# Kernel optimization log

Hardware: AMD Instinct MI355X
Metric: run time of the kernel (lower is better)

Reference implementation:

```python
import jax, jax.numpy as jnp
import numpy as np

IN_SIZE = 32
NUM_ACTIONS = 90
ACTION_DIM = 32
INNER_DIM = 256
HIDDEN_DIM = 512
N_LAYERS = 2
WORLD_STATE_SIZE = 32
# last 8 features are categorical (binary) flags, first 24 numeric
CAT_FLAGS = np.zeros(WORLD_STATE_SIZE, dtype=bool)
CAT_FLAGS[24:] = True


def setup_inputs() -> dict:
    key = jax.random.key(0)
    ks = jax.random.split(key, 20)
    s = 0.05
    b, t = 64, 512
    inp = {
        "batch_world_states_tensor": jax.random.normal(ks[0], (b, t, IN_SIZE), jnp.float32),
        "batch_action_indices": jax.random.randint(ks[1], (b, t), 0, NUM_ACTIONS),
        "action_emb": jax.random.normal(ks[2], (NUM_ACTIONS, ACTION_DIM), jnp.float32),
        "in_w": jax.random.normal(ks[3], (INNER_DIM - ACTION_DIM, IN_SIZE), jnp.float32) * s,
        "in_b": jax.random.normal(ks[4], (INNER_DIM - ACTION_DIM,), jnp.float32) * 0.005,
        "w_ih0": jax.random.normal(ks[5], (4 * HIDDEN_DIM, INNER_DIM), jnp.float32) * s,
        "w_hh0": jax.random.normal(ks[6], (4 * HIDDEN_DIM, HIDDEN_DIM), jnp.float32) * s,
        "b_ih0": jax.random.normal(ks[7], (4 * HIDDEN_DIM,), jnp.float32) * 0.005,
        "b_hh0": jax.random.normal(ks[8], (4 * HIDDEN_DIM,), jnp.float32) * 0.005,
        "w_ih1": jax.random.normal(ks[9], (4 * HIDDEN_DIM, HIDDEN_DIM), jnp.float32) * s,
        "w_hh1": jax.random.normal(ks[10], (4 * HIDDEN_DIM, HIDDEN_DIM), jnp.float32) * s,
        "b_ih1": jax.random.normal(ks[11], (4 * HIDDEN_DIM,), jnp.float32) * 0.005,
        "b_hh1": jax.random.normal(ks[12], (4 * HIDDEN_DIM,), jnp.float32) * 0.005,
        "out_w1": jax.random.normal(ks[13], (2 * HIDDEN_DIM, HIDDEN_DIM), jnp.float32) * s,
        "out_b1": jax.random.normal(ks[14], (2 * HIDDEN_DIM,), jnp.float32) * 0.005,
        "out_w2": jax.random.normal(ks[15], (WORLD_STATE_SIZE, 2 * HIDDEN_DIM), jnp.float32) * s,
        "out_b2": jax.random.normal(ks[16], (WORLD_STATE_SIZE,), jnp.float32) * 0.005,
    }
    return inp


def _lstm_layer(x, w_ih, w_hh, b_ih, b_hh):
    """x: [b, s, d_in] -> ([b, s, H], h_T, c_T). PyTorch gate order i,f,g,o."""
    b = x.shape[0]
    H = w_hh.shape[1]
    # precompute input-to-hidden contributions for all steps: [s, b, 4H]
    gx = jnp.einsum('bsd,gd->sbg', x, w_ih) + b_ih + b_hh
    h0 = jnp.zeros((b, H), x.dtype)
    c0 = jnp.zeros((b, H), x.dtype)

    def step(carry, g_t):
        h, c = carry
        g = g_t + h @ w_hh.T  # [b, 4H]
        i, f, gg, o = jnp.split(g, 4, axis=-1)
        i = jax.nn.sigmoid(i)
        f = jax.nn.sigmoid(f)
        gg = jnp.tanh(gg)
        o = jax.nn.sigmoid(o)
        c = f * c + i * gg
        h = o * jnp.tanh(c)
        return (h, c), h

    (hT, cT), hs = jax.lax.scan(step, (h0, c0), gx)
    return hs.transpose(1, 0, 2), hT, cT  # [b, s, H]


def reference(batch_world_states_tensor, batch_action_indices, action_emb,
              in_w, in_b, w_ih0, w_hh0, b_ih0, b_hh0,
              w_ih1, w_hh1, b_ih1, b_hh1,
              out_w1, out_b1, out_w2, out_b2):
    # input projection + action embedding concat
    proj = jax.nn.relu(jnp.einsum('bsd,ed->bse', batch_world_states_tensor, in_w) + in_b)
    acts = action_emb[batch_action_indices]  # [b, s, action_dim]
    x = jnp.concatenate([proj, acts], axis=-1)  # [b, s, inner_dim]
    # 2-layer LSTM
    x, h0T, c0T = _lstm_layer(x, w_ih0, w_hh0, b_ih0, b_hh0)
    rnn_out, h1T, c1T = _lstm_layer(x, w_ih1, w_hh1, b_ih1, b_hh1)
    # out projector
    hmid = jax.nn.relu(jnp.einsum('bsh,eh->bse', rnn_out, out_w1) + out_b1)
    out = jnp.einsum('bse,de->bsd', hmid, out_w2) + out_b2  # [b, s, D]
    # sigmoid on categorical feature slots
    cat_mask = jnp.asarray(CAT_FLAGS)
    out = jnp.where(cat_mask, jax.nn.sigmoid(out), out)
    return out[:, -1, :]  # [b, D]
```

## Files before the change

### kernel.cpp

```cpp
#include <hip/hip_runtime.h>

#define T_STEPS 512
#define BATCH   64
#define IN_SZ   32
#define AD      32
#define INNER   256
#define PROJ    224
#define HID     512
#define SENTW   0x7F7F7F7Fu
#define DEP     16
#define RST     6
#define SLOTW   4096

typedef __attribute__((ext_vector_type(8))) short short8;
typedef __attribute__((ext_vector_type(4))) float f32x4;
typedef __attribute__((ext_vector_type(4))) int   i32x4;

static __device__ __forceinline__ unsigned short f2bf(float f) {
  unsigned int u = __float_as_uint(f);
  u += 0x7FFFu + ((u >> 16) & 1u);
  return (unsigned short)(u >> 16);
}
static __device__ __forceinline__ float sigmoidf_(float x) { return 1.f / (1.f + __expf(-x)); }
static __device__ __forceinline__ float tanhf_(float x) {
  float e = __expf(-2.f * fabsf(x));
  float r = (1.f - e) / (1.f + e);
  return x < 0.f ? -r : r;
}

__global__ __launch_bounds__(256) void k_prep(
    const float* __restrict__ ws_in, const int* __restrict__ act_idx,
    const float* __restrict__ emb, const float* __restrict__ in_w,
    const float* __restrict__ in_b, unsigned short* __restrict__ x_bf)
{
  int t = blockIdx.x;
  int tid = threadIdx.x;
  __shared__ float st[BATCH * IN_SZ];
  __shared__ int ai[BATCH];
  for (int i = tid; i < BATCH * IN_SZ; i += 256) {
    int b = i >> 5, k = i & 31;
    st[i] = ws_in[((size_t)b * T_STEPS + t) * IN_SZ + k];
  }
  if (tid < BATCH) ai[tid] = act_idx[tid * T_STEPS + t];
  __syncthreads();
  if (tid < PROJ) {
    float w[IN_SZ];
    const float* wrow = in_w + tid * IN_SZ;
#pragma unroll
    for (int k = 0; k < IN_SZ; ++k) w[k] = wrow[k];
    float bb = in_b[tid];
    for (int b = 0; b < BATCH; ++b) {
      float acc = bb;
      const float* sb = st + b * IN_SZ;
#pragma unroll
      for (int k = 0; k < IN_SZ; ++k) acc += w[k] * sb[k];
      x_bf[((size_t)t * BATCH + b) * INNER + tid] = f2bf(fmaxf(acc, 0.f));
    }
  } else {
    int j = tid - PROJ;
    for (int b = 0; b < BATCH; ++b)
      x_bf[((size_t)t * BATCH + b) * INNER + tid] = f2bf(emb[ai[b] * AD + j]);
  }
}

static __device__ __forceinline__ short8 bfrag_load(const float* __restrict__ w, int stride, int row, int k0) {
  const float* p = w + (size_t)row * stride + k0;
  f32x4 a = *reinterpret_cast<const f32x4*>(p);
  f32x4 b = *reinterpret_cast<const f32x4*>(p + 4);
  short8 r;
  r[0] = (short)f2bf(a[0]); r[1] = (short)f2bf(a[1]); r[2] = (short)f2bf(a[2]); r[3] = (short)f2bf(a[3]);
  r[4] = (short)f2bf(b[0]); r[5] = (short)f2bf(b[1]); r[6] = (short)f2bf(b[2]); r[7] = (short)f2bf(b[3]);
  return r;
}

struct Frag64 { unsigned long long u[8]; };
union FU2 { unsigned long long u[2]; short8 s; };

static __device__ __forceinline__ void ld64(const unsigned long long* q, Frag64& f) {
#pragma unroll
  for (int kk = 0; kk < 4; ++kk) {
    f.u[kk * 2]     = __hip_atomic_load(q + kk * 128,     __ATOMIC_RELAXED, __HIP_MEMORY_SCOPE_AGENT);
    f.u[kk * 2 + 1] = __hip_atomic_load(q + kk * 128 + 1, __ATOMIC_RELAXED, __HIP_MEMORY_SCOPE_AGENT);
  }
}
static __device__ __forceinline__ bool fragok(const Frag64& f) {
  bool ok = true;
#pragma unroll
  for (int i = 0; i < 8; ++i)
    ok = ok & ((unsigned)(f.u[i] >> 32) != SENTW) & ((unsigned)f.u[i] != SENTW);
  return ok;
}

static __device__ __forceinline__ Frag64 poll_one(const unsigned long long* q) {
  Frag64 f;
  int miss = 0;
  while (true) {
    ld64(q, f);
    if (__all((int)fragok(f))) break;
    if (++miss > 2) __builtin_amdgcn_s_sleep(1);
  }
  return f;
}
static __device__ __forceinline__ void poll_two(const unsigned long long* qa, const unsigned long long* qb,
                                                Frag64& fa, Frag64& fb) {
  int miss = 0;
  while (true) {
    ld64(qa, fa);
    ld64(qb, fb);
    if (__all((int)(fragok(fa) & fragok(fb)))) break;
    if (++miss > 2) __builtin_amdgcn_s_sleep(1);
  }
}

static __device__ __forceinline__ void mfma4(const Frag64& f, const short8* wf, f32x4* acc) {
#pragma unroll
  for (int kk = 0; kk < 4; ++kk) {
    FU2 u; u.u[0] = f.u[kk * 2]; u.u[1] = f.u[kk * 2 + 1];
#pragma unroll
    for (int g = 0; g < 4; ++g)
      acc[g] = __builtin_amdgcn_mfma_f32_16x16x32_bf16(u.s, wf[g * 4 + kk], acc[g], 0, 0, 0);
  }
}

static __device__ __forceinline__ void st_agent(unsigned int* p, unsigned int v) {
  __hip_atomic_store(p, v, __ATOMIC_RELAXED, __HIP_MEMORY_SCOPE_AGENT);
}

static __device__ __forceinline__ size_t slotw(int bg, int d) { return ((size_t)(bg * DEP + d)) * SLOTW; }

template<int L>
static __device__ void lstm_body(
    const unsigned short* __restrict__ x_bf,
    const float* __restrict__ wih, const float* __restrict__ whh,
    const float* __restrict__ bih, const float* __restrict__ bhh,
    unsigned int* __restrict__ h0w, unsigned int* __restrict__ h1w,
    float* __restrict__ h1fin, unsigned int* __restrict__ flags,
    int bg, int blk, float* __restrict__ spart)
{
  constexpr int KI = (L == 0) ? 2 : 4;

  const int tid  = threadIdx.x;
  const int lane = tid & 63;
  const int wv   = tid >> 6;
  const int q    = lane >> 4;
  const int ln   = lane & 15;
  const int hid0 = blk << 4;
  const int m    = tid >> 4;
  const int n    = tid & 15;
  const int cb64 = (wv * 8 + (q >> 1)) * 64 + ln * 4 + (q & 1) * 2;

  float bias[4];
#pragma unroll
  for (int g = 0; g < 4; ++g)
    bias[g] = bih[g * HID + hid0 + n] + bhh[g * HID + hid0 + n];

  short8 fih[4 * KI];
#pragma unroll
  for (int g = 0; g < 4; ++g)
#pragma unroll
    for (int kk = 0; kk < KI; ++kk)
      fih[g * KI + kk] = bfrag_load(wih, (L == 0) ? INNER : HID,
                                    g * HID + hid0 + ln, (wv * KI + kk) * 32 + q * 8);
  short8 fhh[16];
#pragma unroll
  for (int g = 0; g < 4; ++g)
#pragma unroll
    for (int kk = 0; kk < 4; ++kk)
      fhh[g * 4 + kk] = bfrag_load(whh, HID, g * HID + hid0 + ln, (wv * 4 + kk) * 32 + q * 8);

  const int wo = blk * 128 + m * 8 + (n >> 1);
  float c_state = 0.f;

  for (int t = 0; t < T_STEPS; ++t) {
    f32x4 acc[4];
#pragma unroll
    for (int g = 0; g < 4; ++g) acc[g] = (f32x4){0.f, 0.f, 0.f, 0.f};

    if constexpr (L == 0) {
      const unsigned short* xr = x_bf + ((size_t)t * BATCH + bg * 16 + ln) * INNER + q * 8;
#pragma unroll
      for (int kk = 0; kk < KI; ++kk) {
        short8 xa = *reinterpret_cast<const short8*>(xr + (wv * KI + kk) * 32);
#pragma unroll
        for (int g = 0; g < 4; ++g)
          acc[g] = __builtin_amdgcn_mfma_f32_16x16x32_bf16(xa, fih[g * KI + kk], acc[g], 0, 0, 0);
      }
      if ((t & 3) == 0 && t >= 8) {
        const unsigned int* fp = flags + (bg * 32 + (lane & 31)) * 32;
        unsigned int tgt = (unsigned)(t - 4);
        while (true) {
          unsigned int v = __hip_atomic_load(fp, __ATOMIC_RELAXED, __HIP_MEMORY_SCOPE_AGENT);
          if (__all((int)(v >= tgt))) break;
          __builtin_amdgcn_s_sleep(1);
        }
        asm volatile("" ::: "memory");
      }
      if (t > 0) {
        Frag64 f = poll_one(reinterpret_cast<const unsigned long long*>(h0w + slotw(bg, (t - 1) & (DEP - 1))) + cb64);
        mfma4(f, fhh, acc);
      }
    } else {
      if (t > 0) {
        Frag64 fa, fb;
        poll_two(reinterpret_cast<const unsigned long long*>(h1w + slotw(bg, (t - 1) & (DEP - 1))) + cb64,
                 reinterpret_cast<const unsigned long long*>(h0w + slotw(bg, t & (DEP - 1))) + cb64, fa, fb);
        mfma4(fa, fhh, acc);
        mfma4(fb, fih, acc);
      } else {
        Frag64 fb = poll_one(reinterpret_cast<const unsigned long long*>(h0w + slotw(bg, 0)) + cb64);
        mfma4(fb, fih, acc);
      }
    }

    float* sp_w = spart + (t & 1) * 4096;
#pragma unroll
    for (int g = 0; g < 4; ++g)
#pragma unroll
      for (int r = 0; r < 4; ++r)
        sp_w[(((wv * 4 + g) * 4 + r) * 4 + (q ^ r)) * 16 + ln] = acc[g][r];
    __syncthreads();

    if constexpr (L == 1) {
      if ((t & 1) == 1 && tid == 0)
        st_agent(flags + (bg * 32 + blk) * 32, (unsigned)(t + 1));
    }

    float gate[4];
#pragma unroll
    for (int g = 0; g < 4; ++g) {
      float s = bias[g];
#pragma unroll
      for (int w2 = 0; w2 < 4; ++w2)
        s += sp_w[(((w2 * 4 + g) * 4 + (m & 3)) * 4 + ((m >> 2) ^ (m & 3))) * 16 + n];
      gate[g] = s;
    }
    float gi = sigmoidf_(gate[0]);
    float gf = sigmoidf_(gate[1]);
    float gc = tanhf_(gate[2]);
    float go = sigmoidf_(gate[3]);
    c_state = gf * c_state + gi * gc;
    float h = go * tanhf_(c_state);

    float hp = __shfl_xor(h, 1);
    unsigned int wword = (unsigned)f2bf(h) | ((unsigned)f2bf(hp) << 16);
    if constexpr (L == 0) {
      if (!(n & 1)) {
        st_agent(h0w + slotw(bg, t & (DEP - 1)) + wo, wword);
        st_agent(h0w + slotw(bg, (t + RST) & (DEP - 1)) + wo, SENTW);
      }
    } else {
      if (!(n & 1)) {
        st_agent(h1w + slotw(bg, t & (DEP - 1)) + wo, wword);
        st_agent(h1w + slotw(bg, (t + RST) & (DEP - 1)) + wo, SENTW);
      }
      if (t == T_STEPS - 1)
        h1fin[(size_t)(bg * 16 + m) * HID + hid0 + n] = h;
    }
  }
}

__global__ __launch_bounds__(256, 1) void k_lstm(
    const unsigned short* __restrict__ x_bf,
    const float* __restrict__ w_ih0, const float* __restrict__ w_hh0,
    const float* __restrict__ b_ih0, const float* __restrict__ b_hh0,
    const float* __restrict__ w_ih1, const float* __restrict__ w_hh1,
    const float* __restrict__ b_ih1, const float* __restrict__ b_hh1,
    unsigned int* h0w, unsigned int* h1w, float* h1fin, unsigned int* flags)
{
  __shared__ float spart[2 * 4096];
  const int xg  = blockIdx.x & 7;
  const int blk = blockIdx.x >> 3;
  const int bg  = xg & 3;
  if (xg < 4)
    lstm_body<0>(x_bf, w_ih0, w_hh0, b_ih0, b_hh0, h0w, h1w, h1fin, flags, bg, blk, spart);
  else
    lstm_body<1>(x_bf, w_ih1, w_hh1, b_ih1, b_hh1, h0w, h1w, h1fin, flags, bg, blk, spart);
}

__global__ __launch_bounds__(256) void k_head(
    const float* __restrict__ h1, const float* __restrict__ w1, const float* __restrict__ b1,
    const float* __restrict__ w2, const float* __restrict__ b2, float* __restrict__ out)
{
  int b = blockIdx.x, tid = threadIdx.x;
  __shared__ float sh[HID];
  __shared__ float sm[2 * HID];
  for (int k = tid; k < HID; k += 256) sh[k] = h1[(size_t)b * HID + k];
  __syncthreads();
#pragma unroll
  for (int r0 = 0; r0 < 4; ++r0) {
    int row = r0 * 256 + tid;
    const f32x4* wr = reinterpret_cast<const f32x4*>(w1 + (size_t)row * HID);
    float s = 0.f;
#pragma unroll 4
    for (int k = 0; k < HID / 4; ++k) {
      f32x4 v = wr[k];
      s += v[0] * sh[k * 4] + v[1] * sh[k * 4 + 1] + v[2] * sh[k * 4 + 2] + v[3] * sh[k * 4 + 3];
    }
    sm[row] = fmaxf(b1[row] + s, 0.f);
  }
  __syncthreads();
  if (tid < 32) {
    const f32x4* wr = reinterpret_cast<const f32x4*>(w2 + (size_t)tid * 2 * HID);
    float s = b2[tid];
#pragma unroll 4
    for (int k = 0; k < 2 * HID / 4; ++k) {
      f32x4 v = wr[k];
      s += v[0] * sm[k * 4] + v[1] * sm[k * 4 + 1] + v[2] * sm[k * 4 + 2] + v[3] * sm[k * 4 + 3];
    }
    if (tid >= 24) s = sigmoidf_(s);
    out[b * 32 + tid] = s;
  }
}

extern "C" void kernel_launch(void* const* d_in, const int* in_sizes, int n_in,
                              void* d_out, int out_size, void* d_ws, size_t ws_size,
                              hipStream_t stream) {
  const float* ws_in  = (const float*)d_in[0];
  const int*   aidx   = (const int*)d_in[1];
  const float* emb    = (const float*)d_in[2];
  const float* in_w   = (const float*)d_in[3];
  const float* in_b   = (const float*)d_in[4];
  const float* w_ih0  = (const float*)d_in[5];
  const float* w_hh0  = (const float*)d_in[6];
  const float* b_ih0  = (const float*)d_in[7];
  const float* b_hh0  = (const float*)d_in[8];
  const float* w_ih1  = (const float*)d_in[9];
  const float* w_hh1  = (const float*)d_in[10];
  const float* b_ih1  = (const float*)d_in[11];
  const float* b_hh1  = (const float*)d_in[12];
  const float* out_w1 = (const float*)d_in[13];
  const float* out_b1 = (const float*)d_in[14];
  const float* out_w2 = (const float*)d_in[15];
  const float* out_b2 = (const float*)d_in[16];

  unsigned char* ws = (unsigned char*)d_ws;
  const size_t X_OFF   = 0;
  const size_t RING_SZ = 4u * DEP * SLOTW * 4;
  const size_t H0_OFF  = 16777216;
  const size_t H1_OFF  = H0_OFF + RING_SZ;
  const size_t HF_OFF  = H1_OFF + RING_SZ;
  const size_t FL_OFF  = HF_OFF + 131072;
  unsigned short* x_bf  = (unsigned short*)(ws + X_OFF);
  unsigned int*   h0w   = (unsigned int*)(ws + H0_OFF);
  unsigned int*   h1w   = (unsigned int*)(ws + H1_OFF);
  float*          h1fin = (float*)(ws + HF_OFF);
  unsigned int*   flags = (unsigned int*)(ws + FL_OFF);

  hipMemsetAsync(ws + H0_OFF, 0x7F, 2 * RING_SZ, stream);
  hipMemsetAsync(ws + FL_OFF, 0, 16384, stream);
  k_prep<<<dim3(T_STEPS), dim3(256), 0, stream>>>(ws_in, aidx, emb, in_w, in_b, x_bf);
  k_lstm<<<dim3(256), dim3(256), 0, stream>>>(x_bf, w_ih0, w_hh0, b_ih0, b_hh0,
                                              w_ih1, w_hh1, b_ih1, b_hh1,
                                              h0w, h1w, h1fin, flags);
  k_head<<<dim3(BATCH), dim3(256), 0, stream>>>(h1fin, out_w1, out_b1, out_w2, out_b2, (float*)d_out);
}
```

Before: 1.494 ms.

## Poll per-wave step counters before reading LSTM hidden-state data

Each wave now publishes a step counter after its h stores drain (s_waitcnt vmcnt(0) plus an agent-scope store). Consumers first spin on four small counter words, then read the h fragments, keeping the sentinel check as a fallback. The aim is to replace repeated polling of the full 64-byte data fragments with cheaper polling of counter words, cutting cache and memory traffic while waiting. In exchange it adds a store and a full vmcnt wait per step on the critical recurrent path, plus an extra round-trip between seeing the counter and loading the data.

```diff
diff --git a/kernel.cpp b/kernel.cpp
--- a/kernel.cpp
+++ b/kernel.cpp
@@ -14,7 +14,6 @@
 
 typedef __attribute__((ext_vector_type(8))) short short8;
 typedef __attribute__((ext_vector_type(4))) float f32x4;
-typedef __attribute__((ext_vector_type(4))) int   i32x4;
 
 static __device__ __forceinline__ unsigned short f2bf(float f) {
   unsigned int u = __float_as_uint(f);
@@ -90,8 +89,7 @@
     ok = ok & ((unsigned)(f.u[i] >> 32) != SENTW) & ((unsigned)f.u[i] != SENTW);
   return ok;
 }
-
-static __device__ __forceinline__ Frag64 poll_one(const unsigned long long* q) {
+static __device__ __forceinline__ Frag64 poll_data(const unsigned long long* q) {
   Frag64 f;
   int miss = 0;
   while (true) {
@@ -101,15 +99,31 @@
   }
   return f;
 }
-static __device__ __forceinline__ void poll_two(const unsigned long long* qa, const unsigned long long* qb,
-                                                Frag64& fa, Frag64& fb) {
+
+static __device__ __forceinline__ unsigned ldc(const unsigned int* p) {
+  return __hip_atomic_load(p, __ATOMIC_RELAXED, __HIP_MEMORY_SCOPE_AGENT);
+}
+static __device__ __forceinline__ void poll_can4(const unsigned int* cb, int i0, int i1, int i2, int i3,
+                                                 unsigned tgt) {
   int miss = 0;
   while (true) {
-    ld64(qa, fa);
-    ld64(qb, fb);
-    if (__all((int)(fragok(fa) & fragok(fb)))) break;
-    if (++miss > 2) __builtin_amdgcn_s_sleep(1);
-  }
+    bool ok = (ldc(cb + i0) >= tgt) & (ldc(cb + i1) >= tgt) & (ldc(cb + i2) >= tgt) & (ldc(cb + i3) >= tgt);
+    if (__all((int)ok)) break;
+    if (++miss > 1) __builtin_amdgcn_s_sleep(1);
+  }
+  asm volatile("" ::: "memory");
+}
+static __device__ __forceinline__ void poll_can8(const unsigned int* ca, const unsigned int* cb,
+                                                 int i0, int i1, int i2, int i3,
+                                                 unsigned tga, unsigned tgb) {
+  int miss = 0;
+  while (true) {
+    bool ok = (ldc(ca + i0) >= tga) & (ldc(ca + i1) >= tga) & (ldc(ca + i2) >= tga) & (ldc(ca + i3) >= tga)
+            & (ldc(cb + i0) >= tgb) & (ldc(cb + i1) >= tgb) & (ldc(cb + i2) >= tgb) & (ldc(cb + i3) >= tgb);
+    if (__all((int)ok)) break;
+    if (++miss > 1) __builtin_amdgcn_s_sleep(1);
+  }
+  asm volatile("" ::: "memory");
 }
 
 static __device__ __forceinline__ void mfma4(const Frag64& f, const short8* wf, f32x4* acc) {
@@ -125,7 +139,6 @@
 static __device__ __forceinline__ void st_agent(unsigned int* p, unsigned int v) {
   __hip_atomic_store(p, v, __ATOMIC_RELAXED, __HIP_MEMORY_SCOPE_AGENT);
 }
-
 static __device__ __forceinline__ size_t slotw(int bg, int d) { return ((size_t)(bg * DEP + d)) * SLOTW; }
 
 template<int L>
@@ -135,6 +148,7 @@
     const float* __restrict__ bih, const float* __restrict__ bhh,
     unsigned int* __restrict__ h0w, unsigned int* __restrict__ h1w,
     float* __restrict__ h1fin, unsigned int* __restrict__ flags,
+    unsigned int* __restrict__ can0, unsigned int* __restrict__ can1,
     int bg, int blk, float* __restrict__ spart)
 {
   constexpr int KI = (L == 0) ? 2 : 4;
@@ -148,6 +162,14 @@
   const int m    = tid >> 4;
   const int n    = tid & 15;
   const int cb64 = (wv * 8 + (q >> 1)) * 64 + ln * 4 + (q & 1) * 2;
+  const int pw = ln >> 2;
+  const int ci0 = ((wv * 8 + (q >> 1) + 0) * 4 + pw) * 4;
+  const int ci1 = ((wv * 8 + (q >> 1) + 2) * 4 + pw) * 4;
+  const int ci2 = ((wv * 8 + (q >> 1) + 4) * 4 + pw) * 4;
+  const int ci3 = ((wv * 8 + (q >> 1) + 6) * 4 + pw) * 4;
+  unsigned int* cown = ((L == 0) ? can0 : can1) + bg * 512 + (blk * 4 + wv) * 4;
+  const unsigned int* cg0 = can0 + bg * 512;
+  const unsigned int* cg1 = can1 + bg * 512;
 
   float bias[4];
 #pragma unroll
@@ -196,18 +218,20 @@
         asm volatile("" ::: "memory");
       }
       if (t > 0) {
-        Frag64 f = poll_one(reinterpret_cast<const unsigned long long*>(h0w + slotw(bg, (t - 1) & (DEP - 1))) + cb64);
+        poll_can4(cg0, ci0, ci1, ci2, ci3, (unsigned)t);
+        Frag64 f = poll_data(reinterpret_cast<const unsigned long long*>(h0w + slotw(bg, (t - 1) & (DEP - 1))) + cb64);
         mfma4(f, fhh, acc);
       }
     } else {
       if (t > 0) {
-        Frag64 fa, fb;
-        poll_two(reinterpret_cast<const unsigned long long*>(h1w + slotw(bg, (t - 1) & (DEP - 1))) + cb64,
-                 reinterpret_cast<const unsigned long long*>(h0w + slotw(bg, t & (DEP - 1))) + cb64, fa, fb);
+        poll_can8(cg0, cg1, ci0, ci1, ci2, ci3, (unsigned)(t + 1), (unsigned)t);
+        Frag64 fb = poll_data(reinterpret_cast<const unsigned long long*>(h0w + slotw(bg, t & (DEP - 1))) + cb64);
+        Frag64 fa = poll_data(reinterpret_cast<const unsigned long long*>(h1w + slotw(bg, (t - 1) & (DEP - 1))) + cb64);
+        mfma4(fb, fih, acc);
         mfma4(fa, fhh, acc);
-        mfma4(fb, fih, acc);
       } else {
-        Frag64 fb = poll_one(reinterpret_cast<const unsigned long long*>(h0w + slotw(bg, 0)) + cb64);
+        poll_can4(cg0, ci0, ci1, ci2, ci3, 1u);
+        Frag64 fb = poll_data(reinterpret_cast<const unsigned long long*>(h0w + slotw(bg, 0)) + cb64);
         mfma4(fb, fih, acc);
       }
     }
@@ -256,6 +280,8 @@
       if (t == T_STEPS - 1)
         h1fin[(size_t)(bg * 16 + m) * HID + hid0 + n] = h;
     }
+    asm volatile("s_waitcnt vmcnt(0)" ::: "memory");
+    if (lane == 0) st_agent(cown, (unsigned)(t + 1));
   }
 }
 
@@ -265,16 +291,17 @@
     const float* __restrict__ b_ih0, const float* __restrict__ b_hh0,
     const float* __restrict__ w_ih1, const float* __restrict__ w_hh1,
     const float* __restrict__ b_ih1, const float* __restrict__ b_hh1,
-    unsigned int* h0w, unsigned int* h1w, float* h1fin, unsigned int* flags)
+    unsigned int* h0w, unsigned int* h1w, float* h1fin,
+    unsigned int* flags, unsigned int* can0, unsigned int* can1)
 {
   __shared__ float spart[2 * 4096];
   const int xg  = blockIdx.x & 7;
   const int blk = blockIdx.x >> 3;
   const int bg  = xg & 3;
   if (xg < 4)
-    lstm_body<0>(x_bf, w_ih0, w_hh0, b_ih0, b_hh0, h0w, h1w, h1fin, flags, bg, blk, spart);
+    lstm_body<0>(x_bf, w_ih0, w_hh0, b_ih0, b_hh0, h0w, h1w, h1fin, flags, can0, can1, bg, blk, spart);
   else
-    lstm_body<1>(x_bf, w_ih1, w_hh1, b_ih1, b_hh1, h0w, h1w, h1fin, flags, bg, blk, spart);
+    lstm_body<1>(x_bf, w_ih1, w_hh1, b_ih1, b_hh1, h0w, h1w, h1fin, flags, can0, can1, bg, blk, spart);
 }
 
 __global__ __launch_bounds__(256) void k_head(
@@ -340,17 +367,21 @@
   const size_t H1_OFF  = H0_OFF + RING_SZ;
   const size_t HF_OFF  = H1_OFF + RING_SZ;
   const size_t FL_OFF  = HF_OFF + 131072;
+  const size_t C0_OFF  = FL_OFF + 16384;
+  const size_t C1_OFF  = C0_OFF + 8192;
   unsigned short* x_bf  = (unsigned short*)(ws + X_OFF);
   unsigned int*   h0w   = (unsigned int*)(ws + H0_OFF);
   unsigned int*   h1w   = (unsigned int*)(ws + H1_OFF);
   float*          h1fin = (float*)(ws + HF_OFF);
   unsigned int*   flags = (unsigned int*)(ws + FL_OFF);
+  unsigned int*   can0  = (unsigned int*)(ws + C0_OFF);
+  unsigned int*   can1  = (unsigned int*)(ws + C1_OFF);
 
   hipMemsetAsync(ws + H0_OFF, 0x7F, 2 * RING_SZ, stream);
-  hipMemsetAsync(ws + FL_OFF, 0, 16384, stream);
+  hipMemsetAsync(ws + FL_OFF, 0, 16384 + 8192 + 8192, stream);
   k_prep<<<dim3(T_STEPS), dim3(256), 0, stream>>>(ws_in, aidx, emb, in_w, in_b, x_bf);
   k_lstm<<<dim3(256), dim3(256), 0, stream>>>(x_bf, w_ih0, w_hh0, b_ih0, b_hh0,
                                               w_ih1, w_hh1, b_ih1, b_hh1,
-                                              h0w, h1w, h1fin, flags);
+                                              h0w, h1w, h1fin, flags, can0, can1);
   k_head<<<dim3(BATCH), dim3(256), 0, stream>>>(h1fin, out_w1, out_b1, out_w2, out_b2, (float*)d_out);
 }
```

Measured after the change: 2.314 ms. 54.9% more time.
